# Kernel tuning notes

Measured on AMD Instinct MI355X. Metric: run time of the kernel, lower is better.

## Reference

```python
import jax, jax.numpy as jnp
import numpy as np

D_MODEL = 1024
N_HEAD = 16
N_BR = 4
DH = D_MODEL // N_HEAD            # 64
H_TOT = N_BR * N_HEAD             # 64
SCALE = float(np.pi / np.sqrt(3.0))
ATTN_SCALE = DH ** -0.5


def _rope(x):
    # x: (B, H, T, Dh). Non-interleaved variant: output is cat of the two rotated halves.
    B, H, T, Dh = x.shape
    inv_freq = 1.0 / (10000.0 ** (jnp.arange(0, Dh, 2, dtype=jnp.float32) / Dh))  # (Dh/2,)
    t = jnp.arange(T, dtype=jnp.float32)
    freqs = t[:, None] * inv_freq[None, :]        # (T, Dh/2)
    cos = jnp.cos(freqs)[None, None]              # (1,1,T,Dh/2)
    sin = jnp.sin(freqs)[None, None]
    x1 = x[..., 0::2]
    x2 = x[..., 1::2]
    return jnp.concatenate([-x2 * sin + x1 * cos, x1 * sin + x2 * cos], axis=-1)


def setup_inputs() -> dict:
    key = jax.random.key(0)
    ks = jax.random.split(key, 8)
    s = 0.02
    B, T = 1, 1024
    return {
        "X": jax.random.normal(ks[0], (B, T, D_MODEL), jnp.float32),
        "Wq": jax.random.normal(ks[1], (D_MODEL, H_TOT * DH), jnp.float32) * s,
        "bq": jnp.zeros((H_TOT * DH,), jnp.float32),
        "Wk": jax.random.normal(ks[2], (D_MODEL, D_MODEL), jnp.float32) * s,
        "bk": jnp.zeros((D_MODEL,), jnp.float32),
        "Wv": jax.random.normal(ks[3], (D_MODEL, H_TOT * DH), jnp.float32) * s,
        "bv": jnp.zeros((H_TOT * DH,), jnp.float32),
        "sink_scalars": jax.random.normal(ks[4], (H_TOT, 1, 1), jnp.float32) * s,
        "v_nulls": jax.random.normal(ks[5], (H_TOT, DH), jnp.float32) * s,
        "Wo": jax.random.normal(ks[6], (D_MODEL, D_MODEL), jnp.float32) * s,
        "bo": jnp.zeros((D_MODEL,), jnp.float32),
    }


def reference(X, Wq, bq, Wk, bk, Wv, bv, sink_scalars, v_nulls, Wo, bo):
    B, T, C = X.shape
    q = (X @ Wq + bq).reshape(B, T, H_TOT, DH).transpose(0, 2, 1, 3)   # (B,H,T,Dh)
    v = (X @ Wv + bv).reshape(B, T, H_TOT, DH).transpose(0, 2, 1, 3)
    k_base = (X @ Wk + bk).reshape(B, T, N_HEAD, DH).transpose(0, 2, 1, 3)  # (B,Nh,T,Dh)
    k = jnp.tile(k_base, (1, N_BR, 1, 1))                               # (B,H,T,Dh)

    q = _rope(q)
    k = _rope(k)

    scores = jnp.einsum('bhtd,bhsd->bhts', q, k) * ATTN_SCALE           # (B,H,T,T)
    key_self = jnp.clip(jnp.sum(k * k, axis=-1), 1e-6, None)            # (B,H,T)
    denom = jnp.sqrt(key_self)[:, :, None, :]                           # (B,H,1,T)
    w = jax.nn.softplus(scores / denom)

    causal = jnp.tril(jnp.ones((T, T), dtype=bool))                     # keep lower triangle
    w = jnp.where(causal[None, None], w, 0.0)
    w = w * jax.nn.sigmoid(SCALE * w)

    sinks = jnp.tanh(sink_scalars).reshape(1, H_TOT, 1, 1) + 1e-6       # (1,H,1,1)
    alpha = 1.0 / (jnp.sum(w, axis=-1, keepdims=True) + sinks + 1e-6)   # (B,H,T,1)
    probs_tokens = w * alpha
    probs_sink = sinks * alpha                                          # (B,H,T,1)

    out_tokens = jnp.einsum('bhts,bhsd->bhtd', probs_tokens, v)
    out_sinks = probs_sink * v_nulls[None, :, None, :]                  # (B,H,T,Dh)
    context = out_tokens + out_sinks                                    # (B,H,T,Dh)

    context = context.reshape(B, N_BR, N_HEAD, T, DH)
    context = context.transpose(0, 1, 3, 2, 4).reshape(B, N_BR, T, C)
    y = context @ Wo + bo                                               # (B,N_BR,T,C)
    return jnp.mean(y, axis=1)


if __name__ == "__main__":
    out = reference(**setup_inputs())
    print(out.shape)
```

## Files before the change

kernel.cpp:

```cpp
#include <hip/hip_runtime.h>
#include <math.h>

#define SILU_SCALE 1.8137993642342178f
#define QKV_N 9216
#define LN2 0.6931471805599453f
#define DNSCALE 0.18033688011112042f

typedef __attribute__((ext_vector_type(8))) short bf16x8;
typedef __attribute__((ext_vector_type(4))) float f32x4;

#if __has_builtin(__builtin_amdgcn_exp2f)
#define EXP2(x) __builtin_amdgcn_exp2f(x)
#else
#define EXP2(x) exp2f(x)
#endif
#if __has_builtin(__builtin_amdgcn_logf)
#define LOG2(x) __builtin_amdgcn_logf(x)
#else
#define LOG2(x) __log2f(x)
#endif

__device__ __forceinline__ unsigned short f2bf(float f){
    union { float f; unsigned int i; } u; u.f = f;
    unsigned int r = u.i + 0x7FFFu + ((u.i >> 16) & 1u);
    return (unsigned short)(r >> 16);
}
__device__ __forceinline__ float bf2f(unsigned short s){
    union { unsigned int i; float f; } u; u.i = ((unsigned int)s) << 16;
    return u.f;
}
__device__ __forceinline__ unsigned int pack_bf2(float lo, float hi){
    unsigned int i0 = __float_as_uint(lo) + 0x8000u;
    unsigned int i1 = __float_as_uint(hi) + 0x8000u;
    return __builtin_amdgcn_perm(i1, i0, 0x07060302u);
}

__device__ __forceinline__ void gload_lds16(const void* g, void* l){
    __builtin_amdgcn_global_load_lds(
        (const __attribute__((address_space(1))) void*)g,
        (__attribute__((address_space(3))) void*)l, 16, 0, 0);
}

__global__ __launch_bounds__(256) void prep_kernel(
    const float* __restrict__ X,
    const float* __restrict__ Wq, const float* __restrict__ Wk,
    const float* __restrict__ Wv, const float* __restrict__ Wo,
    const float* __restrict__ bq, const float* __restrict__ bk,
    const float* __restrict__ bv,
    unsigned short* __restrict__ Xb, unsigned short* __restrict__ WqkvT,
    unsigned short* __restrict__ WoT, float* __restrict__ qkvb)
{
    __shared__ float t[64][65];
    int b = blockIdx.x;
    const int tid = threadIdx.x;

    if (b >= 2560){
        if (b < 3072){
            int i = ((b - 2560) * 256 + tid) * 8;
            float4 a = *(const float4*)&X[i];
            float4 c = *(const float4*)&X[i + 4];
            union { unsigned short u[8]; uint4 v; } o;
            o.u[0]=f2bf(a.x); o.u[1]=f2bf(a.y); o.u[2]=f2bf(a.z); o.u[3]=f2bf(a.w);
            o.u[4]=f2bf(c.x); o.u[5]=f2bf(c.y); o.u[6]=f2bf(c.z); o.u[7]=f2bf(c.w);
            *(uint4*)&Xb[i] = o.v;
        } else {
            int i = (b - 3072) * 256 + tid;
            float v;
            if (i < 4096) v = bq[i];
            else if (i < 5120) v = bk[i - 4096];
            else v = bv[i - 5120];
            qkvb[i] = v;
        }
        return;
    }

    const float* W; unsigned short* Wt; int N, tiles_x;
    if (b < 1024)      { W = Wq; Wt = WqkvT;                       N = 4096; tiles_x = 64; }
    else if (b < 1280) { b -= 1024; W = Wk; Wt = WqkvT + (size_t)4096*1024; N = 1024; tiles_x = 16; }
    else if (b < 2304) { b -= 1280; W = Wv; Wt = WqkvT + (size_t)5120*1024; N = 4096; tiles_x = 64; }
    else               { b -= 2304; W = Wo; Wt = WoT;              N = 1024; tiles_x = 16; }

    const int k0 = (b / tiles_x) * 64, n0 = (b % tiles_x) * 64;
    const int lr  = tid >> 4;
    const int lc4 = (tid & 15) * 4;
    #pragma unroll
    for (int p = 0; p < 4; p++){
        int r = lr + p * 16;
        float4 v = *(const float4*)&W[(size_t)(k0 + r) * N + n0 + lc4];
        t[lc4+0][r] = v.x; t[lc4+1][r] = v.y;
        t[lc4+2][r] = v.z; t[lc4+3][r] = v.w;
    }
    __syncthreads();
    const int wr  = tid >> 3;
    const int wc8 = (tid & 7) * 8;
    #pragma unroll
    for (int p = 0; p < 2; p++){
        int r = wr + p * 32;
        union { unsigned short u[8]; uint4 v; } o;
        #pragma unroll
        for (int j = 0; j < 8; j++) o.u[j] = f2bf(t[r][wc8 + j]);
        *(uint4*)&Wt[(size_t)(n0 + r) * 1024 + k0 + wc8] = o.v;
    }
}

template<int BM, int BN, int OUTBF>
__global__ __launch_bounds__(256) void gemm_k(
    const unsigned short* __restrict__ A,
    const unsigned short* __restrict__ Bt,
    const float* __restrict__ bias,
    void* __restrict__ Cout, int M, int N, int K)
{
    constexpr int MT = BM / 32;
    constexpr int NT = BN / 32;
    __shared__ unsigned short As[BM * 64];
    __shared__ unsigned short Bs[BN * 64];
    const int tid  = threadIdx.x;
    const int wave = tid >> 6;
    const int lane = tid & 63;
    const int l15  = lane & 15;
    const int quad = lane >> 4;
    const int m0 = blockIdx.y * BM;
    const int n0 = blockIdx.x * BN;
    const int wm = (wave >> 1) * (BM / 2);
    const int wn = (wave & 1) * (BN / 2);

    f32x4 acc[MT][NT];
    #pragma unroll
    for (int i = 0; i < MT; i++)
        #pragma unroll
        for (int j = 0; j < NT; j++)
            acc[i][j] = (f32x4){0.f, 0.f, 0.f, 0.f};

    for (int k0 = 0; k0 < K; k0 += 64){
        #pragma unroll
        for (int j = 0; j < (BM * 8) / 256; j++){
            int bslot = j * 256 + wave * 64;
            int slot = bslot + lane;
            int row = slot >> 3, phys = slot & 7;
            int c = phys ^ (row & 7);
            gload_lds16(&A[(size_t)(m0 + row) * K + k0 + c * 8], &As[bslot * 8]);
        }
        #pragma unroll
        for (int j = 0; j < (BN * 8) / 256; j++){
            int bslot = j * 256 + wave * 64;
            int slot = bslot + lane;
            int row = slot >> 3, phys = slot & 7;
            int c = phys ^ (row & 7);
            gload_lds16(&Bt[(size_t)(n0 + row) * K + k0 + c * 8], &Bs[bslot * 8]);
        }
        __syncthreads();
        #pragma unroll
        for (int ks = 0; ks < 2; ks++){
            bf16x8 af[MT], bfr[NT];
            #pragma unroll
            for (int i = 0; i < MT; i++){
                int row = wm + i * 16 + l15;
                int phys = (ks * 4 + quad) ^ (row & 7);
                af[i] = *(const bf16x8*)&As[row * 64 + phys * 8];
            }
            #pragma unroll
            for (int j = 0; j < NT; j++){
                int row = wn + j * 16 + l15;
                int phys = (ks * 4 + quad) ^ (row & 7);
                bfr[j] = *(const bf16x8*)&Bs[row * 64 + phys * 8];
            }
            #pragma unroll
            for (int i = 0; i < MT; i++)
                #pragma unroll
                for (int j = 0; j < NT; j++)
                    acc[i][j] = __builtin_amdgcn_mfma_f32_16x16x32_bf16(af[i], bfr[j], acc[i][j], 0, 0, 0);
        }
        __syncthreads();
    }
    #pragma unroll
    for (int i = 0; i < MT; i++){
        #pragma unroll
        for (int j = 0; j < NT; j++){
            int col = n0 + wn + j * 16 + l15;
            float bv = bias[col];
            #pragma unroll
            for (int r = 0; r < 4; r++){
                int row = m0 + wm + i * 16 + quad * 4 + r;
                float v = acc[i][j][r] + bv;
                if (OUTBF) ((unsigned short*)Cout)[(size_t)row * N + col] = f2bf(v);
                else       ((float*)Cout)[(size_t)row * N + col] = v;
            }
        }
    }
}

__global__ __launch_bounds__(256) void gemm_wo(
    const unsigned short* __restrict__ A,
    const unsigned short* __restrict__ Bt,
    float* __restrict__ P)
{
    constexpr int BM = 128, BN = 64, MT = 4, NT = 2;
    __shared__ unsigned short As[BM * 64];
    __shared__ unsigned short Bs[BN * 64];
    const int tid  = threadIdx.x;
    const int wave = tid >> 6;
    const int lane = tid & 63;
    const int l15  = lane & 15;
    const int quad = lane >> 4;
    const int m0 = blockIdx.y * BM;
    const int n0 = blockIdx.x * BN;
    const int kz = blockIdx.z;
    const int wm = (wave >> 1) * 64;
    const int wn = (wave & 1) * 32;

    f32x4 acc[MT][NT];
    #pragma unroll
    for (int i = 0; i < MT; i++)
        #pragma unroll
        for (int j = 0; j < NT; j++)
            acc[i][j] = (f32x4){0.f, 0.f, 0.f, 0.f};

    const int kbeg = kz * 512;
    for (int k0 = kbeg; k0 < kbeg + 512; k0 += 64){
        #pragma unroll
        for (int j = 0; j < (BM * 8) / 256; j++){
            int bslot = j * 256 + wave * 64;
            int slot = bslot + lane;
            int row = slot >> 3, phys = slot & 7;
            int c = phys ^ (row & 7);
            gload_lds16(&A[(size_t)(m0 + row) * 1024 + k0 + c * 8], &As[bslot * 8]);
        }
        #pragma unroll
        for (int j = 0; j < (BN * 8) / 256; j++){
            int bslot = j * 256 + wave * 64;
            int slot = bslot + lane;
            int row = slot >> 3, phys = slot & 7;
            int c = phys ^ (row & 7);
            gload_lds16(&Bt[(size_t)(n0 + row) * 1024 + k0 + c * 8], &Bs[bslot * 8]);
        }
        __syncthreads();
        #pragma unroll
        for (int ks = 0; ks < 2; ks++){
            bf16x8 af[MT], bfr[NT];
            #pragma unroll
            for (int i = 0; i < MT; i++){
                int row = wm + i * 16 + l15;
                int phys = (ks * 4 + quad) ^ (row & 7);
                af[i] = *(const bf16x8*)&As[row * 64 + phys * 8];
            }
            #pragma unroll
            for (int j = 0; j < NT; j++){
                int row = wn + j * 16 + l15;
                int phys = (ks * 4 + quad) ^ (row & 7);
                bfr[j] = *(const bf16x8*)&Bs[row * 64 + phys * 8];
            }
            #pragma unroll
            for (int i = 0; i < MT; i++)
                #pragma unroll
                for (int j = 0; j < NT; j++)
                    acc[i][j] = __builtin_amdgcn_mfma_f32_16x16x32_bf16(af[i], bfr[j], acc[i][j], 0, 0, 0);
        }
        __syncthreads();
    }
    float* Pz = P + (size_t)kz * 1024 * 1024;
    #pragma unroll
    for (int i = 0; i < MT; i++){
        #pragma unroll
        for (int j = 0; j < NT; j++){
            int col = n0 + wn + j * 16 + l15;
            #pragma unroll
            for (int r = 0; r < 4; r++){
                int row = m0 + wm + i * 16 + quad * 4 + r;
                Pz[(size_t)row * 1024 + col] = acc[i][j][r];
            }
        }
    }
}

__global__ void wo_reduce(const float* __restrict__ P, const float* __restrict__ bo,
                          float* __restrict__ out)
{
    int i = (blockIdx.x * 256 + threadIdx.x) * 4;
    float4 a = *(const float4*)&P[i];
    float4 b = *(const float4*)&P[1024 * 1024 + i];
    float4 c = *(const float4*)&bo[i & 1023];
    float4 o;
    o.x = a.x + b.x + c.x; o.y = a.y + b.y + c.y;
    o.z = a.z + b.z + c.z; o.w = a.w + b.w + c.w;
    *(float4*)&out[i] = o;
}

__global__ __launch_bounds__(256) void postproc_kernel(
    unsigned short* __restrict__ qkv, float* __restrict__ dninv,
    unsigned short* __restrict__ VT)
{
    int b = blockIdx.x;
    const int tid = threadIdx.x;
    if (b < 64){
        int idx = b * 256 + tid;
        int t = idx >> 4, h = idx & 15;
        unsigned short* p = qkv + (size_t)t * QKV_N + 4096 + h * 64;
        uint4 raw[8];
        #pragma unroll
        for (int i = 0; i < 8; i++) raw[i] = *(const uint4*)(p + i * 8);
        const unsigned short* rp = (const unsigned short*)raw;
        float x[64];
        #pragma unroll
        for (int i = 0; i < 64; i++) x[i] = bf2f(rp[i]);
        unsigned short o[64];
        float ss = 0.f;
        #pragma unroll
        for (int d = 0; d < 32; d++){
            float inv = EXP2(-(float)d * 0.4152410118609203f);
            float s, c; __sincosf((float)t * inv, &s, &c);
            float x1 = x[2*d], x2 = x[2*d+1];
            float a = x1 * c - x2 * s;
            float bb = x1 * s + x2 * c;
            ss = fmaf(a, a, fmaf(bb, bb, ss));
            o[d]      = f2bf(a);
            o[d + 32] = f2bf(bb);
        }
        #pragma unroll
        for (int i = 0; i < 8; i++) *(uint4*)(p + i * 8) = ((const uint4*)o)[i];
        dninv[h * 1024 + t] = DNSCALE * rsqrtf(fmaxf(ss, 1e-6f));
        return;
    }
    b -= 64;
    const int h = b >> 4, s0 = (b & 15) * 64;
    __shared__ unsigned short tile[64 * 64];
    const unsigned short* V = qkv + 5120;
    const int pr = tid >> 3, cch = tid & 7;
    uint4 g0 = *(const uint4*)&V[(size_t)(s0 + 2 * pr)     * QKV_N + h * 64 + cch * 8];
    uint4 g1 = *(const uint4*)&V[(size_t)(s0 + 2 * pr + 1) * QKV_N + h * 64 + cch * 8];
    const unsigned short* p0 = (const unsigned short*)&g0;
    const unsigned short* p1 = (const unsigned short*)&g1;
    #pragma unroll
    for (int j = 0; j < 8; j++){
        int d = cch * 8 + j;
        int physc = (pr >> 2) ^ ((d ^ (d >> 3)) & 7);
        unsigned int val = (unsigned int)p0[j] | ((unsigned int)p1[j] << 16);
        ((unsigned int*)tile)[d * 32 + physc * 4 + (pr & 3)] = val;
    }
    __syncthreads();
    #pragma unroll
    for (int i = 0; i < 2; i++){
        int slot = tid + i * 256;
        int d = slot >> 3, c = slot & 7;
        int phys = c ^ ((d ^ (d >> 3)) & 7);
        uint4 v = *(const uint4*)&tile[d * 64 + phys * 8];
        *(uint4*)&VT[((size_t)h * 64 + d) * 1024 + s0 + c * 8] = v;
    }
}

__global__ __launch_bounds__(256) void attn_mfma(
    const unsigned short* __restrict__ qkv,
    const unsigned short* __restrict__ VT,
    const float* __restrict__ dninv,
    const float* __restrict__ sinks, const float* __restrict__ vnulls,
    unsigned short* __restrict__ ctx)
{
    __shared__ unsigned short ks[64 * 64];
    __shared__ unsigned short vt[64 * 64];
    __shared__ unsigned short ws[64][72];
    __shared__ float dl[64];
    __shared__ float dsum[4][16];

    const int tid  = threadIdx.x;
    const int wave = tid >> 6;
    const int lane = tid & 63;
    const int l15  = lane & 15;
    const int quad = lane >> 4;
    const int h  = blockIdx.x;
    const int kh = h & 15;
    const int qt = 15 - blockIdx.y;
    const int t0 = qt << 6;

    const unsigned short* Q  = qkv;
    const unsigned short* Kp = qkv + 4096;
    const unsigned short* Vh = VT + (size_t)h * 64 * 1024;

    const int srow0 = tid >> 3,        sphy0 = tid & 7;
    const int srow1 = (tid + 256) >> 3, sphy1 = tid & 7;
    const int sc0 = sphy0 ^ (srow0 & 7);
    const int sc1 = sphy1 ^ (srow1 & 7);

    bf16x8 qf0, qf1;
    {
        const int t = t0 + wave * 16 + l15;
        const unsigned short* qp = Q + (size_t)t * QKV_N + h * 64 + quad * 16;
        uint4 r0 = *(const uint4*)qp;
        uint4 r1 = *(const uint4*)(qp + 8);
        unsigned short e[16];
        *(uint4*)&e[0] = r0; *(uint4*)&e[8] = r1;
        unsigned short o0[8], o1[8];
        #pragma unroll
        for (int j = 0; j < 8; j++){
            int dp = quad * 8 + j;
            float inv = EXP2(-(float)dp * 0.4152410118609203f);
            float s, c; __sincosf((float)t * inv, &s, &c);
            float x1 = bf2f(e[2*j]), x2 = bf2f(e[2*j+1]);
            o0[j] = f2bf(x1 * c - x2 * s);
            o1[j] = f2bf(x1 * s + x2 * c);
        }
        qf0 = *(const bf16x8*)o0;
        qf1 = *(const bf16x8*)o1;
    }

    f32x4 acc_o[4];
    #pragma unroll
    for (int i = 0; i < 4; i++) acc_o[i] = (f32x4){0.f, 0.f, 0.f, 0.f};
    float den = 0.f;
    const int q_glob = t0 + wave * 16 + l15;

    uint4 kr0, kr1, vr0, vr1;
    float dreg = 0.f;
    {
        kr0 = *(const uint4*)&Kp[(size_t)srow0 * QKV_N + kh * 64 + sc0 * 8];
        kr1 = *(const uint4*)&Kp[(size_t)srow1 * QKV_N + kh * 64 + sc1 * 8];
        vr0 = *(const uint4*)&Vh[(size_t)srow0 * 1024 + sc0 * 8];
        vr1 = *(const uint4*)&Vh[(size_t)srow1 * 1024 + sc1 * 8];
        if (tid < 64) dreg = dninv[kh * 1024 + tid];
    }

    for (int st = 0; st <= qt; st++){
        const int s0 = st << 6;
        __syncthreads();

        *(uint4*)&ks[(size_t)tid * 8]         = kr0;
        *(uint4*)&ks[(size_t)(tid + 256) * 8] = kr1;
        *(uint4*)&vt[(size_t)tid * 8]         = vr0;
        *(uint4*)&vt[(size_t)(tid + 256) * 8] = vr1;
        if (tid < 64) dl[tid] = dreg;

        if (st < qt){
            const int sn = (st + 1) << 6;
            kr0 = *(const uint4*)&Kp[(size_t)(sn + srow0) * QKV_N + kh * 64 + sc0 * 8];
            kr1 = *(const uint4*)&Kp[(size_t)(sn + srow1) * QKV_N + kh * 64 + sc1 * 8];
            vr0 = *(const uint4*)&Vh[(size_t)srow0 * 1024 + sn + sc0 * 8];
            vr1 = *(const uint4*)&Vh[(size_t)srow1 * 1024 + sn + sc1 * 8];
            if (tid < 64) dreg = dninv[kh * 1024 + sn + tid];
        }
        __syncthreads();

        const bool diag = (st == qt);

        #pragma unroll
        for (int nt = 0; nt < 4; nt++){
            const int sbase = nt * 16 + quad * 4;
            uint2* wp = (uint2*)&ws[wave * 16 + l15][sbase];
            if (diag && nt > wave){ *wp = (uint2){0u, 0u}; continue; }

            f32x4 sc = (f32x4){0.f, 0.f, 0.f, 0.f};
            {
                int srow = nt * 16 + l15;
                int ph0 = quad ^ (srow & 7);
                int ph1 = (4 + quad) ^ (srow & 7);
                bf16x8 kf0 = *(const bf16x8*)&ks[srow * 64 + ph0 * 8];
                bf16x8 kf1 = *(const bf16x8*)&ks[srow * 64 + ph1 * 8];
                sc = __builtin_amdgcn_mfma_f32_16x16x32_bf16(kf0, qf0, sc, 0, 0, 0);
                sc = __builtin_amdgcn_mfma_f32_16x16x32_bf16(kf1, qf1, sc, 0, 0, 0);
            }
            float da[4];
            *(float4*)da = *(const float4*)&dl[sbase];
            float w4[4];
            #pragma unroll
            for (int r = 0; r < 4; r++){
                float y = sc[r] * da[r];
                float p = EXP2(-fabsf(y));
                float u = fmaxf(y, 0.f) + LOG2(1.f + p);
                float e3 = EXP2(-SILU_SCALE * u);
                float wv = __fdividef(LN2 * u, 1.f + e3);
                wv = (s0 + sbase + r <= q_glob) ? wv : 0.f;
                den += wv;
                w4[r] = wv;
            }
            uint2 pk;
            pk.x = pack_bf2(w4[0], w4[1]);
            pk.y = pack_bf2(w4[2], w4[3]);
            *wp = pk;
        }

        {
            const int prow = wave * 16 + l15;
            bf16x8 pf0 = *(const bf16x8*)&ws[prow][quad * 8];
            bf16x8 pf1 = *(const bf16x8*)&ws[prow][32 + quad * 8];
            const bool skip_hi = diag && (wave <= 1);
            #pragma unroll
            for (int dt = 0; dt < 4; dt++){
                int d = dt * 16 + l15;
                int sw = d & 7;
                bf16x8 vf0 = *(const bf16x8*)&vt[d * 64 + (quad ^ sw) * 8];
                acc_o[dt] = __builtin_amdgcn_mfma_f32_16x16x32_bf16(pf0, vf0, acc_o[dt], 0, 0, 0);
                if (!skip_hi){
                    bf16x8 vf1 = *(const bf16x8*)&vt[d * 64 + ((4 + quad) ^ sw) * 8];
                    acc_o[dt] = __builtin_amdgcn_mfma_f32_16x16x32_bf16(pf1, vf1, acc_o[dt], 0, 0, 0);
                }
            }
        }
    }

    den += __shfl_xor(den, 16);
    den += __shfl_xor(den, 32);
    if (quad == 0) dsum[wave][l15] = den;
    float den4[4];
    *(float4*)den4 = *(const float4*)&dsum[wave][quad * 4];

    float sinkv = tanhf(sinks[h]) + 1e-6f;
    #pragma unroll
    for (int r = 0; r < 4; r++){
        int qg = t0 + wave * 16 + quad * 4 + r;
        float alpha = __fdividef(1.f, den4[r] + sinkv + 1e-6f);
        #pragma unroll
        for (int dt = 0; dt < 4; dt++){
            int d = dt * 16 + l15;
            float o = (acc_o[dt][r] + sinkv * vnulls[h * 64 + d]) * alpha;
            ctx[((size_t)h * 1024 + qg) * 64 + d] = f2bf(o);
        }
    }
}

__global__ void avg_kernel(const unsigned short* __restrict__ ctx, unsigned short* __restrict__ avg)
{
    int i8 = (blockIdx.x * 256 + threadIdx.x) * 8;
    int t = i8 >> 10, c = i8 & 1023;
    int nh = c >> 6, d = c & 63;
    float s[8] = {};
    #pragma unroll
    for (int br = 0; br < 4; br++){
        uint4 v = *(const uint4*)&ctx[((size_t)(br * 16 + nh) * 1024 + t) * 64 + d];
        const unsigned short* p = (const unsigned short*)&v;
        #pragma unroll
        for (int j = 0; j < 8; j++) s[j] += bf2f(p[j]);
    }
    union { unsigned short u[8]; uint4 v; } o;
    #pragma unroll
    for (int j = 0; j < 8; j++) o.u[j] = f2bf(0.25f * s[j]);
    *(uint4*)&avg[i8] = o.v;
}

extern "C" void kernel_launch(void* const* d_in, const int* in_sizes, int n_in,
                              void* d_out, int out_size, void* d_ws, size_t ws_size,
                              hipStream_t stream)
{
    (void)in_sizes; (void)n_in; (void)out_size; (void)ws_size;
    const float* X      = (const float*)d_in[0];
    const float* Wq     = (const float*)d_in[1];
    const float* bq     = (const float*)d_in[2];
    const float* Wk     = (const float*)d_in[3];
    const float* bk     = (const float*)d_in[4];
    const float* Wv     = (const float*)d_in[5];
    const float* bv     = (const float*)d_in[6];
    const float* sinks  = (const float*)d_in[7];
    const float* vnulls = (const float*)d_in[8];
    const float* Wo     = (const float*)d_in[9];
    const float* bo     = (const float*)d_in[10];
    float* out = (float*)d_out;

    unsigned short* w16   = (unsigned short*)d_ws;
    unsigned short* Xb    = w16;
    unsigned short* WqkvT = Xb    + (size_t)1024 * 1024;
    unsigned short* QKVb  = WqkvT + (size_t)QKV_N * 1024;
    unsigned short* WoT   = QKVb  + (size_t)1024 * QKV_N;
    unsigned short* ctxb  = WoT   + (size_t)1024 * 1024;
    unsigned short* avgb  = ctxb  + (size_t)64 * 1024 * 64;
    float* qkvb = (float*)(avgb + (size_t)1024 * 1024);
    float* dnf  = qkvb + QKV_N;
    unsigned short* VTb = WqkvT;
    float* pWo = (float*)(WqkvT + (size_t)4 * 1024 * 1024);

    dim3 blk(256);
    prep_kernel<<<3108, blk, 0, stream>>>(X, Wq, Wk, Wv, Wo, bq, bk, bv,
                                          Xb, WqkvT, WoT, qkvb);
    gemm_k<128, 96, 1><<<dim3(96, 8), blk, 0, stream>>>(Xb, WqkvT, qkvb, QKVb, 1024, QKV_N, 1024);
    postproc_kernel<<<1088, blk, 0, stream>>>(QKVb, dnf, VTb);
    attn_mfma<<<dim3(64, 16), blk, 0, stream>>>(QKVb, VTb, dnf, sinks, vnulls, ctxb);
    avg_kernel<<<512, blk, 0, stream>>>(ctxb, avgb);
    gemm_wo<<<dim3(16, 8, 2), blk, 0, stream>>>(avgb, WoT, pWo);
    wo_reduce<<<1024, blk, 0, stream>>>(pWo, bo, out);
}
```

Measured before the change: 192.4 us.

## Split attention key range across two blocks and combine partials in averaging kernel

```diff
diff --git a/kernel.cpp b/kernel.cpp
--- a/kernel.cpp
+++ b/kernel.cpp
@@ -351,14 +351,13 @@
     const unsigned short* __restrict__ qkv,
     const unsigned short* __restrict__ VT,
     const float* __restrict__ dninv,
-    const float* __restrict__ sinks, const float* __restrict__ vnulls,
-    unsigned short* __restrict__ ctx)
+    unsigned short* __restrict__ num0, unsigned short* __restrict__ num1,
+    float* __restrict__ den0, float* __restrict__ den1)
 {
     __shared__ unsigned short ks[64 * 64];
     __shared__ unsigned short vt[64 * 64];
     __shared__ unsigned short ws[64][72];
     __shared__ float dl[64];
-    __shared__ float dsum[4][16];
 
     const int tid  = threadIdx.x;
     const int wave = tid >> 6;
@@ -367,14 +366,19 @@
     const int quad = lane >> 4;
     const int h  = blockIdx.x;
     const int kh = h & 15;
-    const int qt = 15 - blockIdx.y;
+    const int yy = blockIdx.y;
+    const int qt = 15 - (yy >> 1);
+    const int z  = yy & 1;
     const int t0 = qt << 6;
+    const int nh0 = (qt + 2) >> 1;
+    const int st_begin = z ? nh0 : 0;
+    const int st_end   = z ? (qt + 1) : nh0;
 
     const unsigned short* Q  = qkv;
     const unsigned short* Kp = qkv + 4096;
     const unsigned short* Vh = VT + (size_t)h * 64 * 1024;
 
-    const int srow0 = tid >> 3,        sphy0 = tid & 7;
+    const int srow0 = tid >> 3,         sphy0 = tid & 7;
     const int srow1 = (tid + 256) >> 3, sphy1 = tid & 7;
     const int sc0 = sphy0 ^ (srow0 & 7);
     const int sc1 = sphy1 ^ (srow1 & 7);
@@ -407,17 +411,18 @@
     float den = 0.f;
     const int q_glob = t0 + wave * 16 + l15;
 
-    uint4 kr0, kr1, vr0, vr1;
+    uint4 kr0 = {}, kr1 = {}, vr0 = {}, vr1 = {};
     float dreg = 0.f;
-    {
-        kr0 = *(const uint4*)&Kp[(size_t)srow0 * QKV_N + kh * 64 + sc0 * 8];
-        kr1 = *(const uint4*)&Kp[(size_t)srow1 * QKV_N + kh * 64 + sc1 * 8];
-        vr0 = *(const uint4*)&Vh[(size_t)srow0 * 1024 + sc0 * 8];
-        vr1 = *(const uint4*)&Vh[(size_t)srow1 * 1024 + sc1 * 8];
-        if (tid < 64) dreg = dninv[kh * 1024 + tid];
-    }
-
-    for (int st = 0; st <= qt; st++){
+    if (st_begin < st_end){
+        const int sb = st_begin << 6;
+        kr0 = *(const uint4*)&Kp[(size_t)(sb + srow0) * QKV_N + kh * 64 + sc0 * 8];
+        kr1 = *(const uint4*)&Kp[(size_t)(sb + srow1) * QKV_N + kh * 64 + sc1 * 8];
+        vr0 = *(const uint4*)&Vh[(size_t)srow0 * 1024 + sb + sc0 * 8];
+        vr1 = *(const uint4*)&Vh[(size_t)srow1 * 1024 + sb + sc1 * 8];
+        if (tid < 64) dreg = dninv[kh * 1024 + sb + tid];
+    }
+
+    for (int st = st_begin; st < st_end; st++){
         const int s0 = st << 6;
         __syncthreads();
 
@@ -427,7 +432,7 @@
         *(uint4*)&vt[(size_t)(tid + 256) * 8] = vr1;
         if (tid < 64) dl[tid] = dreg;
 
-        if (st < qt){
+        if (st + 1 < st_end){
             const int sn = (st + 1) << 6;
             kr0 = *(const uint4*)&Kp[(size_t)(sn + srow0) * QKV_N + kh * 64 + sc0 * 8];
             kr1 = *(const uint4*)&Kp[(size_t)(sn + srow1) * QKV_N + kh * 64 + sc1 * 8];
@@ -496,36 +501,43 @@
 
     den += __shfl_xor(den, 16);
     den += __shfl_xor(den, 32);
-    if (quad == 0) dsum[wave][l15] = den;
-    float den4[4];
-    *(float4*)den4 = *(const float4*)&dsum[wave][quad * 4];
-
-    float sinkv = tanhf(sinks[h]) + 1e-6f;
+    unsigned short* numZ = z ? num1 : num0;
+    float* denZ = z ? den1 : den0;
+    if (quad == 0) denZ[h * 1024 + t0 + wave * 16 + l15] = den;
     #pragma unroll
     for (int r = 0; r < 4; r++){
         int qg = t0 + wave * 16 + quad * 4 + r;
-        float alpha = __fdividef(1.f, den4[r] + sinkv + 1e-6f);
         #pragma unroll
         for (int dt = 0; dt < 4; dt++){
             int d = dt * 16 + l15;
-            float o = (acc_o[dt][r] + sinkv * vnulls[h * 64 + d]) * alpha;
-            ctx[((size_t)h * 1024 + qg) * 64 + d] = f2bf(o);
-        }
-    }
-}
-
-__global__ void avg_kernel(const unsigned short* __restrict__ ctx, unsigned short* __restrict__ avg)
+            numZ[((size_t)h * 1024 + qg) * 64 + d] = f2bf(acc_o[dt][r]);
+        }
+    }
+}
+
+__global__ void combine_avg(
+    const unsigned short* __restrict__ num0, const unsigned short* __restrict__ num1,
+    const float* __restrict__ den0, const float* __restrict__ den1,
+    const float* __restrict__ sinks, const float* __restrict__ vnulls,
+    unsigned short* __restrict__ avg)
 {
     int i8 = (blockIdx.x * 256 + threadIdx.x) * 8;
     int t = i8 >> 10, c = i8 & 1023;
-    int nh = c >> 6, d = c & 63;
+    int nh = c >> 6, d0 = c & 63;
     float s[8] = {};
     #pragma unroll
     for (int br = 0; br < 4; br++){
-        uint4 v = *(const uint4*)&ctx[((size_t)(br * 16 + nh) * 1024 + t) * 64 + d];
-        const unsigned short* p = (const unsigned short*)&v;
-        #pragma unroll
-        for (int j = 0; j < 8; j++) s[j] += bf2f(p[j]);
+        int h = br * 16 + nh;
+        size_t base = ((size_t)h * 1024 + t) * 64 + d0;
+        uint4 a = *(const uint4*)&num0[base];
+        uint4 b = *(const uint4*)&num1[base];
+        const unsigned short* pa = (const unsigned short*)&a;
+        const unsigned short* pb = (const unsigned short*)&b;
+        float sink = tanhf(sinks[h]) + 1e-6f;
+        float alpha = __fdividef(1.f, den0[h * 1024 + t] + den1[h * 1024 + t] + sink + 1e-6f);
+        #pragma unroll
+        for (int j = 0; j < 8; j++)
+            s[j] += (bf2f(pa[j]) + bf2f(pb[j]) + sink * vnulls[h * 64 + d0 + j]) * alpha;
     }
     union { unsigned short u[8]; uint4 v; } o;
     #pragma unroll
@@ -560,16 +572,20 @@
     unsigned short* avgb  = ctxb  + (size_t)64 * 1024 * 64;
     float* qkvb = (float*)(avgb + (size_t)1024 * 1024);
     float* dnf  = qkvb + QKV_N;
-    unsigned short* VTb = WqkvT;
-    float* pWo = (float*)(WqkvT + (size_t)4 * 1024 * 1024);
+    unsigned short* VTb  = WqkvT;
+    unsigned short* num0 = WqkvT + (size_t)4 * 1024 * 1024;
+    unsigned short* num1 = ctxb;
+    float* den0 = (float*)Xb;
+    float* den1 = den0 + 64 * 1024;
+    float* pWo  = (float*)num0;
 
     dim3 blk(256);
     prep_kernel<<<3108, blk, 0, stream>>>(X, Wq, Wk, Wv, Wo, bq, bk, bv,
                                           Xb, WqkvT, WoT, qkvb);
     gemm_k<128, 96, 1><<<dim3(96, 8), blk, 0, stream>>>(Xb, WqkvT, qkvb, QKVb, 1024, QKV_N, 1024);
     postproc_kernel<<<1088, blk, 0, stream>>>(QKVb, dnf, VTb);
-    attn_mfma<<<dim3(64, 16), blk, 0, stream>>>(QKVb, VTb, dnf, sinks, vnulls, ctxb);
-    avg_kernel<<<512, blk, 0, stream>>>(ctxb, avgb);
+    attn_mfma<<<dim3(64, 32), blk, 0, stream>>>(QKVb, VTb, dnf, num0, num1, den0, den1);
+    combine_avg<<<512, blk, 0, stream>>>(num0, num1, den0, den1, sinks, vnulls, avgb);
     gemm_wo<<<dim3(16, 8, 2), blk, 0, stream>>>(avgb, WoT, pWo);
     wo_reduce<<<1024, blk, 0, stream>>>(pWo, bo, out);
 }
```

Measured after the change: 193.1 us. About the same (+0.4%).
